# Kernel optimization log

Measured on AMD Instinct MI355X. Metric: run time of the kernel, lower is better.

## Reference

```python
import jax, jax.numpy as jnp
import numpy as np

NUM_TAGS = 64
HIDDEN = 768
INTERMEDIATE = 3072
TAGGING_RATE = 1.0
LN_EPS = 1e-12


def layer_norm(x, g, b):
    mu = jnp.mean(x, axis=-1, keepdims=True)
    var = jnp.mean(jnp.square(x - mu), axis=-1, keepdims=True)
    return (x - mu) * jax.lax.rsqrt(var + LN_EPS) * g + b


def setup_inputs() -> dict:
    key = jax.random.key(0)
    ks = jax.random.split(key, 16)
    B, S, H, I = 8, 4096, HIDDEN, INTERMEDIATE
    s = 0.02
    return {
        "word_embedding": jax.random.normal(ks[0], (B, S, H), jnp.float32),
        "token_tags": jax.random.randint(ks[1], (B, S), 0, NUM_TAGS, jnp.int32),
        "tag_mask": jax.random.randint(ks[2], (B, S), 0, 2, jnp.int32),
        # learned params
        "tag_emb": jax.random.normal(ks[3], (NUM_TAGS, H), jnp.float32) * s,
        "Wv": jax.random.normal(ks[4], (H, H), jnp.float32) * s,   # v_proj (applied as x @ Wv)
        "bv": jnp.zeros((H,), jnp.float32),
        "Wo": jax.random.normal(ks[5], (H, H), jnp.float32) * s,   # out_proj
        "bo": jnp.zeros((H,), jnp.float32),
        "ln1_g": jnp.ones((H,), jnp.float32),
        "ln1_b": jnp.zeros((H,), jnp.float32),
        "W1": jax.random.normal(ks[6], (H, I), jnp.float32) * s,
        "b1": jnp.zeros((I,), jnp.float32),
        "W2": jax.random.normal(ks[7], (I, H), jnp.float32) * s,
        "b2": jnp.zeros((H,), jnp.float32),
        "ln2_g": jnp.ones((H,), jnp.float32),
        "ln2_b": jnp.zeros((H,), jnp.float32),
    }


def reference(word_embedding, token_tags, tag_mask, tag_emb, Wv, bv, Wo, bo,
              ln1_g, ln1_b, W1, b1, W2, b2, ln2_g, ln2_b):
    # MHA with a single key/value: softmax over one key == 1 for every head,
    # so attention_output = out_proj(v_proj(tag_embedding[tag])), independent of q.
    per_tag = (tag_emb @ Wv + bv) @ Wo + bo              # [num_tags, H]
    taged = per_tag[token_tags] * tag_mask[..., None].astype(word_embedding.dtype)  # [B,S,H]
    x = word_embedding + taged * TAGGING_RATE            # dropout is identity in eval
    x = layer_norm(x, ln1_g, ln1_b)
    ff = jax.nn.relu(x @ W1 + b1) @ W2 + b2              # feed_forward
    out = layer_norm(ff + x, ln2_g, ln2_b)
    return out
```

## Files before the change

kernel.cpp:

```cpp
#include <hip/hip_runtime.h>
#include <hip/hip_bf16.h>
#include <cstdint>
#include <cstddef>

typedef __hip_bfloat16 bf16;
typedef __attribute__((ext_vector_type(8))) short short8;
typedef __attribute__((ext_vector_type(4))) float f32x4;

__device__ __forceinline__ void gload_lds16(const void* g, void* l) {
    __builtin_amdgcn_global_load_lds((const __attribute__((address_space(1))) void*)g,
                                     (__attribute__((address_space(3))) void*)l,
                                     16, 0, 0);
}

__global__ __launch_bounds__(256)
void transpose_cvt(const float* __restrict__ in, bf16* __restrict__ out, int R, int C)
{
    __shared__ float tile[32][33];
    const int tx = threadIdx.x & 31;
    const int ty = threadIdx.x >> 5;
    const int c0 = blockIdx.x * 32;
    const int r0 = blockIdx.y * 32;
    #pragma unroll
    for (int j = 0; j < 32; j += 8)
        tile[ty + j][tx] = in[(size_t)(r0 + ty + j) * C + c0 + tx];
    __syncthreads();
    #pragma unroll
    for (int j = 0; j < 32; j += 8)
        out[(size_t)(c0 + ty + j) * R + r0 + tx] = __float2bfloat16(tile[tx][ty + j]);
}

__global__ __launch_bounds__(256)
void tag_gemm_a(const float* __restrict__ te, const float* __restrict__ Wv,
                const float* __restrict__ bv, float* __restrict__ t1)
{
    const int idx = blockIdx.x * 256 + threadIdx.x;
    const int i = idx / 768, j = idx - i * 768;
    float acc = bv[j];
    const float* a = te + (size_t)i * 768;
    for (int k = 0; k < 768; ++k)
        acc += a[k] * Wv[(size_t)k * 768 + j];
    t1[idx] = acc;
}

__global__ __launch_bounds__(256)
void tag_gemm_b(const float* __restrict__ t1, const float* __restrict__ Wo,
                const float* __restrict__ bo, float* __restrict__ ptab)
{
    const int idx = blockIdx.x * 256 + threadIdx.x;
    const int i = idx / 768, j = idx - i * 768;
    float acc = bo[j];
    const float* a = t1 + (size_t)i * 768;
    for (int k = 0; k < 768; ++k)
        acc += a[k] * Wo[(size_t)k * 768 + j];
    ptab[idx] = acc;
}

__global__ __launch_bounds__(256)
void addtag_ln(const float* __restrict__ we, const int* __restrict__ tags,
               const int* __restrict__ mask, const float* __restrict__ ptab,
               const float* __restrict__ g, const float* __restrict__ b,
               bf16* __restrict__ out)
{
    const int row = blockIdx.x;
    const int t = threadIdx.x;
    const int lane = t & 63, wid = t >> 6;
    const int tag = tags[row];
    const float msk = (float)mask[row];
    const float* wr = we + (size_t)row * 768;
    const float* pt = ptab + (size_t)tag * 768;
    float x[3];
    float s = 0.f, s2 = 0.f;
    #pragma unroll
    for (int j = 0; j < 3; ++j) {
        const int c = t + j * 256;
        const float v = wr[c] + msk * pt[c];
        x[j] = v; s += v; s2 += v * v;
    }
    #pragma unroll
    for (int o = 32; o > 0; o >>= 1) { s += __shfl_down(s, o); s2 += __shfl_down(s2, o); }
    __shared__ float ls[4], ls2[4];
    if (lane == 0) { ls[wid] = s; ls2[wid] = s2; }
    __syncthreads();
    s  = ls[0] + ls[1] + ls[2] + ls[3];
    s2 = ls2[0] + ls2[1] + ls2[2] + ls2[3];
    const float mean = s * (1.f / 768.f);
    float var = s2 * (1.f / 768.f) - mean * mean;
    var = var < 0.f ? 0.f : var;
    const float inv = 1.f / sqrtf(var + 1e-12f);
    bf16* orow = out + (size_t)row * 768;
    #pragma unroll
    for (int j = 0; j < 3; ++j) {
        const int c = t + j * 256;
        orow[c] = __float2bfloat16((x[j] - mean) * inv * g[c] + b[c]);
    }
}

__global__ __launch_bounds__(256)
void ln_inplace(float* __restrict__ y, const float* __restrict__ g, const float* __restrict__ b)
{
    const int row = blockIdx.x;
    const int t = threadIdx.x;
    const int lane = t & 63, wid = t >> 6;
    float* yr = y + (size_t)row * 768;
    float x[3];
    float s = 0.f, s2 = 0.f;
    #pragma unroll
    for (int j = 0; j < 3; ++j) {
        const int c = t + j * 256;
        const float v = yr[c];
        x[j] = v; s += v; s2 += v * v;
    }
    #pragma unroll
    for (int o = 32; o > 0; o >>= 1) { s += __shfl_down(s, o); s2 += __shfl_down(s2, o); }
    __shared__ float ls[4], ls2[4];
    if (lane == 0) { ls[wid] = s; ls2[wid] = s2; }
    __syncthreads();
    s  = ls[0] + ls[1] + ls[2] + ls[3];
    s2 = ls2[0] + ls2[1] + ls2[2] + ls2[3];
    const float mean = s * (1.f / 768.f);
    float var = s2 * (1.f / 768.f) - mean * mean;
    var = var < 0.f ? 0.f : var;
    const float inv = 1.f / sqrtf(var + 1e-12f);
    #pragma unroll
    for (int j = 0; j < 3; ++j) {
        const int c = t + j * 256;
        yr[c] = (x[j] - mean) * inv * g[c] + b[c];
    }
}

template<int EPI, typename OutT>
__global__ __launch_bounds__(256)
void gemm128(const bf16* __restrict__ A, const bf16* __restrict__ Bt,
             const float* __restrict__ bias, const bf16* __restrict__ resid,
             OutT* __restrict__ C, int N, int K)
{
    __shared__ bf16 As[128 * 64];
    __shared__ bf16 Bs[128 * 64];
    const int t = threadIdx.x;
    const int lane = t & 63;
    const int wid  = t >> 6;
    const int quad = lane >> 4;
    const int lr   = lane & 15;
    const int rowBase = blockIdx.y * 128;
    const int colBase = blockIdx.x * 128;
    const int wm = (wid >> 1) * 64;
    const int wn = (wid & 1) * 64;

    f32x4 acc[4][4] = {};

    const char* Ab = (const char*)(A + (size_t)rowBase * K);
    const char* Bb = (const char*)(Bt + (size_t)colBase * K);
    const int strideBytes = K * 2;
    char* AsB = (char*)As;
    char* BsB = (char*)Bs;

    int srow[4], soff[4];
    #pragma unroll
    for (int p = 0; p < 4; ++p) {
        const int i = t + p * 256;
        srow[p] = i >> 3;
        soff[p] = ((i & 7) ^ (srow[p] & 7)) * 16;
    }

    for (int kt = 0; kt < K; kt += 64) {
        const int kb = kt * 2;
        #pragma unroll
        for (int p = 0; p < 4; ++p) {
            const int i = t + p * 256;
            gload_lds16(Ab + (size_t)srow[p] * strideBytes + kb + soff[p], AsB + i * 16);
            gload_lds16(Bb + (size_t)srow[p] * strideBytes + kb + soff[p], BsB + i * 16);
        }
        __syncthreads();
        #pragma unroll
        for (int j = 0; j < 2; ++j) {
            const int cch = j * 4 + quad;
            short8 af[4], bfr[4];
            #pragma unroll
            for (int mi = 0; mi < 4; ++mi) {
                const int R = wm + mi * 16 + lr;
                af[mi] = *(const short8*)(AsB + R * 128 + ((cch ^ (R & 7)) * 16));
            }
            #pragma unroll
            for (int ni = 0; ni < 4; ++ni) {
                const int R = wn + ni * 16 + lr;
                bfr[ni] = *(const short8*)(BsB + R * 128 + ((cch ^ (R & 7)) * 16));
            }
            #pragma unroll
            for (int mi = 0; mi < 4; ++mi) {
                #pragma unroll
                for (int ni = 0; ni < 4; ++ni)
                    acc[mi][ni] = __builtin_amdgcn_mfma_f32_16x16x32_bf16(
                        af[mi], bfr[ni], acc[mi][ni], 0, 0, 0);
            }
        }
        __syncthreads();
    }

    #pragma unroll
    for (int ni = 0; ni < 4; ++ni) {
        const int gc = colBase + wn + ni * 16 + lr;
        const float bvv = bias[gc];
        #pragma unroll
        for (int mi = 0; mi < 4; ++mi) {
            const int gr0 = rowBase + wm + mi * 16 + quad * 4;
            #pragma unroll
            for (int r = 0; r < 4; ++r) {
                const size_t off = (size_t)(gr0 + r) * N + gc;
                float v = acc[mi][ni][r] + bvv;
                if (EPI == 0) {
                    v = v > 0.f ? v : 0.f;
                    C[off] = (OutT)__float2bfloat16(v);
                } else {
                    v += (float)resid[off];
                    C[off] = (OutT)v;
                }
            }
        }
    }
}

extern "C" void kernel_launch(void* const* d_in, const int* in_sizes, int n_in,
                              void* d_out, int out_size, void* d_ws, size_t ws_size,
                              hipStream_t stream)
{
    const float* we      = (const float*)d_in[0];
    const int*   tags    = (const int*)d_in[1];
    const int*   mask    = (const int*)d_in[2];
    const float* tag_emb = (const float*)d_in[3];
    const float* Wv      = (const float*)d_in[4];
    const float* bv      = (const float*)d_in[5];
    const float* Wo      = (const float*)d_in[6];
    const float* bo      = (const float*)d_in[7];
    const float* ln1g    = (const float*)d_in[8];
    const float* ln1b    = (const float*)d_in[9];
    const float* W1      = (const float*)d_in[10];
    const float* b1      = (const float*)d_in[11];
    const float* W2      = (const float*)d_in[12];
    const float* b2      = (const float*)d_in[13];
    const float* ln2g    = (const float*)d_in[14];
    const float* ln2b    = (const float*)d_in[15];
    float* out = (float*)d_out;

    const int M = 8 * 4096;
    char* ws = (char*)d_ws;
    const size_t oT1   = 0;
    const size_t oPtab = 196608;
    const size_t oW1t  = 393216;
    const size_t oW2t  = 5111808;
    const size_t oXn   = 9830400;
    const size_t oHh   = 60162048;
    const size_t hhFull = (size_t)M * 3072 * 2;

    const int nchunk = (ws_size >= oHh + hhFull) ? 1 : 2;
    const int MC = M / nchunk;

    float* t1   = (float*)(ws + oT1);
    float* ptab = (float*)(ws + oPtab);
    bf16*  W1t  = (bf16*)(ws + oW1t);
    bf16*  W2t  = (bf16*)(ws + oW2t);
    bf16*  xn   = (bf16*)(ws + oXn);
    bf16*  hh   = (bf16*)(ws + oHh);

    transpose_cvt<<<dim3(3072 / 32, 768 / 32), 256, 0, stream>>>(W1, W1t, 768, 3072);
    transpose_cvt<<<dim3(768 / 32, 3072 / 32), 256, 0, stream>>>(W2, W2t, 3072, 768);

    tag_gemm_a<<<192, 256, 0, stream>>>(tag_emb, Wv, bv, t1);
    tag_gemm_b<<<192, 256, 0, stream>>>(t1, Wo, bo, ptab);

    addtag_ln<<<M, 256, 0, stream>>>(we, tags, mask, ptab, ln1g, ln1b, xn);

    for (int c = 0; c < nchunk; ++c) {
        const bf16* xnC = xn + (size_t)c * MC * 768;
        gemm128<0, bf16><<<dim3(3072 / 128, MC / 128), 256, 0, stream>>>(
            xnC, W1t, b1, nullptr, hh, 3072, 768);
        gemm128<1, float><<<dim3(768 / 128, MC / 128), 256, 0, stream>>>(
            hh, W2t, b2, xnC, out + (size_t)c * MC * 768, 768, 3072);
    }

    ln_inplace<<<M, 256, 0, stream>>>(out, ln2g, ln2b);
}
```

Before: 823.3 us.

## Replace 128x128 GEMM with 256x256 double-buffered pipelined MFMA kernel

Both FFN GEMMs move from a 128x128 tile with 256 threads and a single LDS buffer to a 256x256 tile with 512 threads and 128KB of double-buffered dynamic LDS. Global-to-LDS loads for the next k-tiles are interleaved with MFMA work using explicit vmcnt/lgkmcnt waits, raw barriers and setprio. The 1D grid is remapped with an XCD-aware swizzle to improve L2 reuse. The larger tile raises register pressure, and the hand-ordered waits and barriers are fragile if the load counts are off.

```diff
diff --git a/kernel.cpp b/kernel.cpp
--- a/kernel.cpp
+++ b/kernel.cpp
@@ -12,6 +12,11 @@
                                      (__attribute__((address_space(3))) void*)l,
                                      16, 0, 0);
 }
+
+__device__ __forceinline__ void vm_wait6() { asm volatile("s_waitcnt vmcnt(6)" ::: "memory"); }
+__device__ __forceinline__ void vm_wait0() { asm volatile("s_waitcnt vmcnt(0)" ::: "memory"); }
+#define SBAR  asm volatile("s_barrier" ::: "memory")
+#define LGKM0 asm volatile("s_waitcnt lgkmcnt(0)" ::: "memory")
 
 __global__ __launch_bounds__(256)
 void transpose_cvt(const float* __restrict__ in, bf16* __restrict__ out, int R, int C)
@@ -130,80 +135,119 @@
 }
 
 template<int EPI, typename OutT>
-__global__ __launch_bounds__(256)
-void gemm128(const bf16* __restrict__ A, const bf16* __restrict__ Bt,
+__global__ __launch_bounds__(512, 2)
+void gemm256(const bf16* __restrict__ A, const bf16* __restrict__ Bt,
              const float* __restrict__ bias, const bf16* __restrict__ resid,
-             OutT* __restrict__ C, int N, int K)
-{
-    __shared__ bf16 As[128 * 64];
-    __shared__ bf16 Bs[128 * 64];
-    const int t = threadIdx.x;
+             OutT* __restrict__ C, int N, int K, int nbx)
+{
+    extern __shared__ char smem[];
+    char* const AsB = smem;
+    char* const BsB = smem + 65536;
+
+    const int t    = threadIdx.x;
     const int lane = t & 63;
     const int wid  = t >> 6;
     const int quad = lane >> 4;
     const int lr   = lane & 15;
-    const int rowBase = blockIdx.y * 128;
-    const int colBase = blockIdx.x * 128;
-    const int wm = (wid >> 1) * 64;
-    const int wn = (wid & 1) * 64;
-
-    f32x4 acc[4][4] = {};
-
-    const char* Ab = (const char*)(A + (size_t)rowBase * K);
-    const char* Bb = (const char*)(Bt + (size_t)colBase * K);
-    const int strideBytes = K * 2;
-    char* AsB = (char*)As;
-    char* BsB = (char*)Bs;
-
-    int srow[4], soff[4];
-    #pragma unroll
-    for (int p = 0; p < 4; ++p) {
-        const int i = t + p * 256;
-        srow[p] = i >> 3;
-        soff[p] = ((i & 7) ^ (srow[p] & 7)) * 16;
-    }
-
-    for (int kt = 0; kt < K; kt += 64) {
-        const int kb = kt * 2;
-        #pragma unroll
-        for (int p = 0; p < 4; ++p) {
-            const int i = t + p * 256;
-            gload_lds16(Ab + (size_t)srow[p] * strideBytes + kb + soff[p], AsB + i * 16);
-            gload_lds16(Bb + (size_t)srow[p] * strideBytes + kb + soff[p], BsB + i * 16);
-        }
-        __syncthreads();
-        #pragma unroll
-        for (int j = 0; j < 2; ++j) {
-            const int cch = j * 4 + quad;
-            short8 af[4], bfr[4];
-            #pragma unroll
-            for (int mi = 0; mi < 4; ++mi) {
-                const int R = wm + mi * 16 + lr;
-                af[mi] = *(const short8*)(AsB + R * 128 + ((cch ^ (R & 7)) * 16));
-            }
-            #pragma unroll
-            for (int ni = 0; ni < 4; ++ni) {
-                const int R = wn + ni * 16 + lr;
-                bfr[ni] = *(const short8*)(BsB + R * 128 + ((cch ^ (R & 7)) * 16));
-            }
-            #pragma unroll
-            for (int mi = 0; mi < 4; ++mi) {
-                #pragma unroll
-                for (int ni = 0; ni < 4; ++ni)
-                    acc[mi][ni] = __builtin_amdgcn_mfma_f32_16x16x32_bf16(
-                        af[mi], bfr[ni], acc[mi][ni], 0, 0, 0);
-            }
-        }
-        __syncthreads();
+    const int wmRow = (wid >> 2) * 128;
+    const int wnRow = (wid & 3) * 64;
+
+    const int nwg = gridDim.x;
+    const int swz = (blockIdx.x & 7) * (nwg >> 3) + (blockIdx.x >> 3);
+    const int bx = swz % nbx;
+    const int by = swz / nbx;
+    const int rowBase = by * 256;
+    const int colBase = bx * 256;
+
+    const char* const Ab = (const char*)(A + (size_t)rowBase * K);
+    const char* const Bb = (const char*)(Bt + (size_t)colBase * K);
+    const int strideB = K * 2;
+    const int nkt = K >> 6;
+
+    f32x4 acc[8][4] = {};
+
+    const int i0 = t, i1 = t + 512;
+    const int r0 = i0 >> 3, r1 = i1 >> 3;
+    const int sc0 = ((i0 & 7) ^ (r0 & 7)) * 16;
+    const int sc1 = ((i1 & 7) ^ (r1 & 7)) * 16;
+
+    #define STAGE_A(buf_, kt_, h_) do {                                          \
+        const int kb_ = (kt_) * 128;                                             \
+        gload_lds16(Ab + (size_t)((h_)*128 + r0) * strideB + kb_ + sc0,          \
+                    AsB + (buf_)*32768 + (h_)*16384 + i0*16);                    \
+        gload_lds16(Ab + (size_t)((h_)*128 + r1) * strideB + kb_ + sc1,          \
+                    AsB + (buf_)*32768 + (h_)*16384 + i1*16);                    \
+    } while (0)
+    #define STAGE_B(buf_, kt_, h_) do {                                          \
+        const int kb_ = (kt_) * 128;                                             \
+        gload_lds16(Bb + (size_t)((h_)*128 + r0) * strideB + kb_ + sc0,          \
+                    BsB + (buf_)*32768 + (h_)*16384 + i0*16);                    \
+        gload_lds16(Bb + (size_t)((h_)*128 + r1) * strideB + kb_ + sc1,          \
+                    BsB + (buf_)*32768 + (h_)*16384 + i1*16);                    \
+    } while (0)
+
+    short8 af0[8], af1[8], bf0[4], bf1[4];
+    #define RD_A(buf_, ks_, dst_) do {                                           \
+        const int cch_ = (ks_)*4 + quad;                                         \
+        _Pragma("unroll")                                                        \
+        for (int mi = 0; mi < 8; ++mi) {                                         \
+            const int R_ = wmRow + mi*16 + lr;                                   \
+            dst_[mi] = *(const short8*)(AsB + (buf_)*32768 + R_*128 +            \
+                                        ((cch_ ^ (R_ & 7)) * 16));               \
+        }                                                                        \
+    } while (0)
+    #define RD_B(buf_, ks_, dst_) do {                                           \
+        const int cch_ = (ks_)*4 + quad;                                         \
+        _Pragma("unroll")                                                        \
+        for (int ni = 0; ni < 4; ++ni) {                                         \
+            const int R_ = wnRow + ni*16 + lr;                                   \
+            dst_[ni] = *(const short8*)(BsB + (buf_)*32768 + R_*128 +            \
+                                        ((cch_ ^ (R_ & 7)) * 16));               \
+        }                                                                        \
+    } while (0)
+    #define MFMA8x2(AF_, BF_, n0_) do {                                          \
+        __builtin_amdgcn_s_setprio(1);                                           \
+        _Pragma("unroll")                                                        \
+        for (int mi = 0; mi < 8; ++mi) {                                         \
+            acc[mi][(n0_)]   = __builtin_amdgcn_mfma_f32_16x16x32_bf16(          \
+                AF_[mi], BF_[(n0_)],   acc[mi][(n0_)],   0, 0, 0);               \
+            acc[mi][(n0_)+1] = __builtin_amdgcn_mfma_f32_16x16x32_bf16(          \
+                AF_[mi], BF_[(n0_)+1], acc[mi][(n0_)+1], 0, 0, 0);               \
+        }                                                                        \
+        __builtin_amdgcn_s_setprio(0);                                           \
+    } while (0)
+
+    STAGE_A(0, 0, 0); STAGE_A(0, 0, 1); STAGE_B(0, 0, 0); STAGE_B(0, 0, 1);
+    if (nkt > 1) { STAGE_A(1, 1, 0); STAGE_A(1, 1, 1); STAGE_B(1, 1, 0); }
+
+    for (int kt = 0; kt < nkt; ++kt) {
+        const int buf = kt & 1;
+        if (kt == nkt - 1) vm_wait0(); else vm_wait6();
+        SBAR;
+        RD_A(buf, 0, af0);
+        RD_B(buf, 0, bf0);
+        if (kt + 1 < nkt) STAGE_B(buf ^ 1, kt + 1, 1);
+        MFMA8x2(af0, bf0, 0);
+        SBAR;
+        RD_A(buf, 1, af1);
+        RD_B(buf, 1, bf1);
+        MFMA8x2(af0, bf0, 2);
+        LGKM0;
+        SBAR;
+        if (kt + 2 < nkt) { STAGE_A(buf, kt + 2, 0); STAGE_A(buf, kt + 2, 1); }
+        MFMA8x2(af1, bf1, 0);
+        SBAR;
+        if (kt + 2 < nkt) STAGE_B(buf, kt + 2, 0);
+        MFMA8x2(af1, bf1, 2);
     }
 
     #pragma unroll
     for (int ni = 0; ni < 4; ++ni) {
-        const int gc = colBase + wn + ni * 16 + lr;
+        const int gc = colBase + wnRow + ni * 16 + lr;
         const float bvv = bias[gc];
         #pragma unroll
-        for (int mi = 0; mi < 4; ++mi) {
-            const int gr0 = rowBase + wm + mi * 16 + quad * 4;
+        for (int mi = 0; mi < 8; ++mi) {
+            const int gr0 = rowBase + wmRow + mi * 16 + quad * 4;
             #pragma unroll
             for (int r = 0; r < 4; ++r) {
                 const size_t off = (size_t)(gr0 + r) * N + gc;
@@ -218,6 +262,11 @@
             }
         }
     }
+    #undef STAGE_A
+    #undef STAGE_B
+    #undef RD_A
+    #undef RD_B
+    #undef MFMA8x2
 }
 
 extern "C" void kernel_launch(void* const* d_in, const int* in_sizes, int n_in,
@@ -242,6 +291,15 @@
     const float* ln2b    = (const float*)d_in[15];
     float* out = (float*)d_out;
 
+    static bool attr_set = false;
+    if (!attr_set) {
+        hipFuncSetAttribute(reinterpret_cast<const void*>(&gemm256<0, bf16>),
+                            hipFuncAttributeMaxDynamicSharedMemorySize, 131072);
+        hipFuncSetAttribute(reinterpret_cast<const void*>(&gemm256<1, float>),
+                            hipFuncAttributeMaxDynamicSharedMemorySize, 131072);
+        attr_set = true;
+    }
+
     const int M = 8 * 4096;
     char* ws = (char*)d_ws;
     const size_t oT1   = 0;
@@ -272,10 +330,11 @@
 
     for (int c = 0; c < nchunk; ++c) {
         const bf16* xnC = xn + (size_t)c * MC * 768;
-        gemm128<0, bf16><<<dim3(3072 / 128, MC / 128), 256, 0, stream>>>(
-            xnC, W1t, b1, nullptr, hh, 3072, 768);
-        gemm128<1, float><<<dim3(768 / 128, MC / 128), 256, 0, stream>>>(
-            hh, W2t, b2, xnC, out + (size_t)c * MC * 768, 768, 3072);
+        const int nby = MC / 256;
+        gemm256<0, bf16><<<(3072 / 256) * nby, 512, 131072, stream>>>(
+            xnC, W1t, b1, nullptr, hh, 3072, 768, 3072 / 256);
+        gemm256<1, float><<<(768 / 256) * nby, 512, 131072, stream>>>(
+            hh, W2t, b2, xnC, out + (size_t)c * MC * 768, 768, 3072, 768 / 256);
     }
 
     ln_inplace<<<M, 256, 0, stream>>>(out, ln2g, ln2b);
```

Result: faster. 757.7 us (-8.0%).
